# Kernel optimization log

Hardware: AMD Instinct MI355X
Metric: run time of the kernel (lower is better)

## Reference

```python
import jax, jax.numpy as jnp
import numpy as np

N_NODES = 40000
N_EDGES = 640000
IN_CH = 128
HID = 128
OUT_CH = 16
N_GRAPHS = 64
EPS = 1e-16


def segment_softmax(logits, seg, num_segments):
    m = jax.ops.segment_max(logits, seg, num_segments=num_segments)
    e = jnp.exp(logits - m[seg])
    s = jax.ops.segment_sum(e, seg, num_segments=num_segments)
    return e / (s[seg] + EPS)


def gt_conv(x, src, dst, W, b, att):
    # x: [N, Cin] -> h: [N, C]
    h = x @ W + b
    s = h @ att  # [N] per-node attention score (att broadcast over rows)
    # alpha_e = <x_i, att> + <x_j, att>; x_i = target (dst), x_j = source (src)
    alpha = s[dst] + s[src]
    alpha = jax.nn.leaky_relu(alpha, negative_slope=0.2)
    # PyG code normalizes over edge_index[0] groups (source nodes)
    alpha = segment_softmax(alpha, src, x.shape[0])
    msg = h[src] * alpha[:, None]
    return jax.ops.segment_sum(msg, dst, num_segments=x.shape[0])


def gcn_conv(x, src, dst, W, b):
    n = x.shape[0]
    h = x @ W
    deg = jax.ops.segment_sum(jnp.ones_like(src, dtype=h.dtype), dst, num_segments=n)
    dinv = jnp.where(deg > 0, deg ** -0.5, 0.0)
    norm = dinv[src] * dinv[dst]
    out = jax.ops.segment_sum(h[src] * norm[:, None], dst, num_segments=n)
    return out + b


def setup_inputs() -> dict:
    key = jax.random.key(0)
    ks = jax.random.split(key, 12)
    x = jax.random.normal(ks[0], (N_NODES, IN_CH), dtype=jnp.float32)
    edge_index = jax.random.randint(ks[1], (2, N_EDGES), 0, N_NODES, dtype=jnp.int32)
    batch = jnp.sort(jax.random.randint(ks[2], (N_NODES,), 0, N_GRAPHS, dtype=jnp.int32))
    def glorot(k, shape):
        fan_in, fan_out = shape[0], shape[-1]
        lim = jnp.sqrt(6.0 / (fan_in + fan_out))
        return jax.random.uniform(k, shape, jnp.float32, -lim, lim)
    return {
        "x": x, "edge_index": edge_index, "batch": batch,
        "W1": glorot(ks[3], (IN_CH, HID)), "b1": jnp.zeros((HID,), jnp.float32),
        "att1": glorot(ks[4], (1, HID))[0],
        "W2": glorot(ks[5], (HID, HID)), "b2": jnp.zeros((HID,), jnp.float32),
        "att2": glorot(ks[6], (1, HID))[0],
        "Wg": glorot(ks[7], (HID, HID)), "bg": jnp.zeros((HID,), jnp.float32),
        "Wfc": glorot(ks[8], (HID, OUT_CH)), "bfc": jnp.zeros((OUT_CH,), jnp.float32),
    }


def reference(x, edge_index, batch, W1, b1, att1, W2, b2, att2, Wg, bg, Wfc, bfc):
    n = x.shape[0]
    loops = jnp.arange(n, dtype=edge_index.dtype)
    src = jnp.concatenate([edge_index[0], loops])
    dst = jnp.concatenate([edge_index[1], loops])
    # two GT layers (dropout is identity in eval mode)
    h = jax.nn.relu(gt_conv(x, src, dst, W1, b1, att1))
    h = jax.nn.relu(gt_conv(h, src, dst, W2, b2, att2))
    # GCNConv (with self loops, symmetric normalization)
    h = gcn_conv(h, src, dst, Wg, bg)
    # global mean pool over graphs
    sums = jax.ops.segment_sum(h, batch, num_segments=N_GRAPHS)
    counts = jax.ops.segment_sum(jnp.ones((n,), h.dtype), batch, num_segments=N_GRAPHS)
    pooled = sums / jnp.maximum(counts, 1.0)[:, None]
    logits = pooled @ Wfc + bfc
    return jax.nn.log_softmax(logits, axis=1)
```

## Files before the change

kernel.cpp:

```cpp
#include <hip/hip_runtime.h>
#include <hip/hip_fp16.h>
#include <hip/hip_fp8.h>
#include <math.h>

#define NN 40000
#define NE 640000
#define ET 680000
#define CH 128
#define OC 16
#define NG 64
#define NQ (ET/4)
#define CAP 48
#define NBKT 8
#define BKT_DIV 5000
#define NFILLB 5320
#define NGEMMB 625
#define NGRP 79
#define GRP 72
#define NBLK1 (NGRP*GRP + (NFILLB - NGRP*64))

typedef _Float16 h8 __attribute__((ext_vector_type(8)));
typedef float    f4 __attribute__((ext_vector_type(4)));

__device__ __forceinline__ float2 fp8x2_to_f32(unsigned short v) {
    __hip_fp8_e4m3 a, b;
    a.__x = (__hip_fp8_storage_t)(v & 0xff);
    b.__x = (__hip_fp8_storage_t)(v >> 8);
    return make_float2((float)a, (float)b);
}
__device__ __forceinline__ unsigned char f32_to_fp8(float f) {
    __hip_fp8_e4m3 t(f);
    return (unsigned char)t.__x;
}

__global__ __launch_bounds__(256)
void prep(const int* __restrict__ batch, int* __restrict__ gstart,
          int* __restrict__ cur_d, int* __restrict__ cur_s,
          float* __restrict__ pooled,
          const float* __restrict__ W1, const float* __restrict__ W2,
          const float* __restrict__ Wg, _Float16* __restrict__ Wt1,
          _Float16* __restrict__ Wt2, _Float16* __restrict__ Wtg)
{
    int i = blockIdx.x * 256 + threadIdx.x;
    if (i < NN) {
        cur_d[i] = 0; cur_s[i] = 0;
        int b = batch[i];
        if (i == 0) { for (int g = 0; g <= b; ++g) gstart[g] = 0; }
        else { int pb = batch[i - 1]; for (int g = pb + 1; g <= b; ++g) gstart[g] = i; }
        if (i == NN - 1) { for (int g = b + 1; g <= NG; ++g) gstart[g] = NN; }
    }
    if (i < NG * CH) pooled[i] = 0.f;
    if (i < CH * CH) {
        int k = i >> 7, n = i & 127;
        Wt1[n * CH + k] = (_Float16)W1[i];
        Wt2[n * CH + k] = (_Float16)W2[i];
        Wtg[n * CH + k] = (_Float16)Wg[i];
    }
}

template<bool RELU, bool BIAS, bool ATTN, bool IN16>
__device__ __forceinline__
void gemm_tile(_Float16 (*xs)[136], const void* __restrict__ in_,
               const _Float16* __restrict__ Wt, const float* __restrict__ bias,
               const float* __restrict__ att, unsigned char* __restrict__ out8,
               float* __restrict__ s, int rb, int tid)
{
    if (IN16) {
        const __half* in = (const __half*)in_;
#pragma unroll
        for (int i = 0; i < 4; ++i) {
            int f = tid + i * 256;
            int r = f >> 4, c8 = f & 15;
            float4 raw = *(const float4*)(in + (size_t)(rb + r) * CH + c8 * 8);
            if (RELU) {
                __half2* h2 = (__half2*)&raw;
#pragma unroll
                for (int u = 0; u < 4; ++u) {
                    float2 fv = __half22float2(h2[u]);
                    h2[u] = __floats2half2_rn(fmaxf(fv.x, 0.f), fmaxf(fv.y, 0.f));
                }
            }
            *(float4*)&xs[r][c8 * 8] = raw;
        }
    } else {
        const float* in = (const float*)in_;
#pragma unroll
        for (int i = 0; i < 4; ++i) {
            int f = tid + i * 256;
            int r = f >> 4, c8 = f & 15;
            const float* p = in + (size_t)(rb + r) * CH + c8 * 8;
            float4 v0 = *(const float4*)p;
            float4 v1 = *(const float4*)(p + 4);
            if (RELU) {
                v0.x=fmaxf(v0.x,0.f); v0.y=fmaxf(v0.y,0.f); v0.z=fmaxf(v0.z,0.f); v0.w=fmaxf(v0.w,0.f);
                v1.x=fmaxf(v1.x,0.f); v1.y=fmaxf(v1.y,0.f); v1.z=fmaxf(v1.z,0.f); v1.w=fmaxf(v1.w,0.f);
            }
            __half2 h[4] = { __floats2half2_rn(v0.x, v0.y), __floats2half2_rn(v0.z, v0.w),
                             __floats2half2_rn(v1.x, v1.y), __floats2half2_rn(v1.z, v1.w) };
            *(float4*)&xs[r][c8 * 8] = *(float4*)h;
        }
    }
    __syncthreads();
    const int wv = tid >> 6, lane = tid & 63;
    const int m = lane & 15, quad = lane >> 4;
    f4 acc[8] = {};
    const _Float16* wp = Wt + (size_t)m * CH + quad * 8;
#pragma unroll
    for (int ks = 0; ks < 4; ++ks) {
        h8 a = *(const h8*)&xs[wv * 16 + m][ks * 32 + quad * 8];
#pragma unroll
        for (int t = 0; t < 8; ++t) {
            h8 b = *(const h8*)(wp + (size_t)t * 16 * CH + ks * 32);
            acc[t] = __builtin_amdgcn_mfma_f32_16x16x32_f16(a, b, acc[t], 0, 0, 0);
        }
    }
    float pr[4] = {0.f, 0.f, 0.f, 0.f};
#pragma unroll
    for (int t = 0; t < 8; ++t) {
        int col = t * 16 + m;
        float bv = BIAS ? bias[col] : 0.f;
        float av = ATTN ? att[col] : 0.f;
#pragma unroll
        for (int r = 0; r < 4; ++r) {
            float o = acc[t][r] + bv;
            int row = rb + wv * 16 + quad * 4 + r;
            out8[(size_t)row * CH + col] = f32_to_fp8(o);
            if (ATTN) pr[r] += o * av;
        }
    }
    if (ATTN) {
#pragma unroll
        for (int r = 0; r < 4; ++r) {
            float p = pr[r];
            p += __shfl_xor(p, 1); p += __shfl_xor(p, 2);
            p += __shfl_xor(p, 4); p += __shfl_xor(p, 8);
            if (m == 0) s[rb + wv * 16 + quad * 4 + r] = p;
        }
    }
}

__device__ __forceinline__
void fill_body(int fb, int tid, const int* __restrict__ ei,
               int* __restrict__ cur_d, int* __restrict__ cur_s,
               unsigned short* __restrict__ pad_src,
               unsigned short* __restrict__ pad_dst)
{
    int bkt = fb & (NBKT - 1);
    int q = (fb >> 3) * 256 + tid;
    if (q >= NQ) return;
    int e0 = q * 4;
    int4 sv, dv;
    if (e0 < NE) {
        sv = *(const int4*)(ei + e0);
        dv = *(const int4*)(ei + NE + e0);
    } else {
        int b = e0 - NE;
        sv = make_int4(b, b + 1, b + 2, b + 3);
        dv = sv;
    }
    const int* sc = (const int*)&sv;
    const int* dc = (const int*)&dv;
#pragma unroll
    for (int u = 0; u < 4; ++u) {
        int srcE = sc[u], dstE = dc[u];
        if ((unsigned)dstE / BKT_DIV == (unsigned)bkt) {
            int p = atomicAdd(cur_d + dstE, 1);
            if (p < CAP) pad_src[dstE * CAP + p] = (unsigned short)srcE;
        }
        if ((unsigned)srcE / BKT_DIV == (unsigned)bkt) {
            int p = atomicAdd(cur_s + srcE, 1);
            if (p < CAP) pad_dst[srcE * CAP + p] = (unsigned short)dstE;
        }
    }
}

__global__ __launch_bounds__(256)
void fill_gemm1(const float* __restrict__ x, const _Float16* __restrict__ Wt1,
                const float* __restrict__ b1, const float* __restrict__ att1,
                unsigned char* __restrict__ A8, float* __restrict__ s1,
                const int* __restrict__ ei, int* __restrict__ cur_d,
                int* __restrict__ cur_s, unsigned short* __restrict__ pad_src,
                unsigned short* __restrict__ pad_dst)
{
    __shared__ __attribute__((aligned(16))) _Float16 xs[64][136];
    int grp = blockIdx.x / GRP, o = blockIdx.x % GRP;
    if (grp < NGRP && o < 8) {
        int g = grp * 8 + o;
        if (g < NGEMMB)
            gemm_tile<false, true, true, false>(xs, x, Wt1, b1, att1,
                                                A8, s1, g * 64, threadIdx.x);
        return;
    }
    int fb = (grp < NGRP) ? grp * 64 + (o - 8)
                          : NGRP * 64 + (blockIdx.x - NGRP * GRP);
    if (fb < NFILLB)
        fill_body(fb, threadIdx.x, ei, cur_d, cur_s, pad_src, pad_dst);
}

template<bool RELU, bool BIAS, bool ATTN, bool IN16>
__global__ __launch_bounds__(256)
void gemm_k(const void* __restrict__ in_, const _Float16* __restrict__ Wt,
            const float* __restrict__ bias, const float* __restrict__ att,
            unsigned char* __restrict__ out8, float* __restrict__ s)
{
    __shared__ __attribute__((aligned(16))) _Float16 xs[64][136];
    gemm_tile<RELU, BIAS, ATTN, IN16>(xs, in_, Wt, bias, att, out8, s,
                                      blockIdx.x * 64, threadIdx.x);
}

__global__ __launch_bounds__(256)
void softmax_stats(const int* __restrict__ cur_s,
                   const unsigned short* __restrict__ pad_dst,
                   const float* __restrict__ s, float* __restrict__ ssum)
{
    int node = (blockIdx.x * 256 + threadIdx.x) >> 6;
    int lane = threadIdx.x & 63;
    if (node >= NN) return;
    int deg = min(cur_s[node], CAP);
    float si = s[node];
    float sum = 0.f;
    if (lane < deg) {
        int d = pad_dst[node * CAP + lane];
        float t = si + s[d];
        t = t > 0.f ? t : 0.2f * t;
        sum = expf(t);
    }
#pragma unroll
    for (int o = 32; o; o >>= 1) sum += __shfl_xor(sum, o);
    if (lane == 0) ssum[node] = sum;
}

__device__ __forceinline__
void gather_core(int node, int lane, int deg, int src, float w,
                 const unsigned char* __restrict__ h8p, __half* __restrict__ out16)
{
    int qtr = lane >> 4, cl = lane & 15;
    float a[8] = {};
    for (int base = 0; base < deg; base += 8) {
        uint2 v[2]; float wj[2];
#pragma unroll
        for (int u = 0; u < 2; ++u) {
            int e = base + 4 * u + qtr;
            int sj = __shfl(src, e);
            wj[u]  = __shfl(w, e);
            v[u] = ((const uint2*)(h8p + (size_t)sj * CH))[cl];
        }
#pragma unroll
        for (int u = 0; u < 2; ++u) {
            float2 p0 = fp8x2_to_f32((unsigned short)(v[u].x & 0xffff));
            float2 p1 = fp8x2_to_f32((unsigned short)(v[u].x >> 16));
            float2 p2 = fp8x2_to_f32((unsigned short)(v[u].y & 0xffff));
            float2 p3 = fp8x2_to_f32((unsigned short)(v[u].y >> 16));
            a[0] += p0.x * wj[u]; a[1] += p0.y * wj[u];
            a[2] += p1.x * wj[u]; a[3] += p1.y * wj[u];
            a[4] += p2.x * wj[u]; a[5] += p2.y * wj[u];
            a[6] += p3.x * wj[u]; a[7] += p3.y * wj[u];
        }
    }
#pragma unroll
    for (int k = 0; k < 8; ++k) {
        a[k] += __shfl_xor(a[k], 16);
        a[k] += __shfl_xor(a[k], 32);
    }
    if (qtr == 0) {
        float4 st;
        ((__half2*)&st)[0] = __floats2half2_rn(a[0], a[1]);
        ((__half2*)&st)[1] = __floats2half2_rn(a[2], a[3]);
        ((__half2*)&st)[2] = __floats2half2_rn(a[4], a[5]);
        ((__half2*)&st)[3] = __floats2half2_rn(a[6], a[7]);
        ((float4*)(out16 + (size_t)node * CH))[cl] = st;
    }
}

__global__ __launch_bounds__(256)
void gt_gather(const int* __restrict__ cur_d,
               const unsigned short* __restrict__ pad_src,
               const unsigned char* __restrict__ h8p, const float* __restrict__ s,
               const float* __restrict__ ssum, __half* __restrict__ out16)
{
    int node = (blockIdx.x * 256 + threadIdx.x) >> 6;
    int lane = threadIdx.x & 63;
    if (node >= NN) return;
    int deg = min(cur_d[node], CAP);
    float sd = s[node];
    int src = 0; float w = 0.f;
    if (lane < deg) {
        src = pad_src[node * CAP + lane];
        float t = sd + s[src];
        t = t > 0.f ? t : 0.2f * t;
        w = expf(t) / ssum[src];
    }
    gather_core(node, lane, deg, src, w, h8p, out16);
}

__global__ __launch_bounds__(256)
void gcn_gather(const int* __restrict__ cur_d,
                const unsigned short* __restrict__ pad_src,
                const unsigned char* __restrict__ h8p, __half* __restrict__ out16)
{
    int node = (blockIdx.x * 256 + threadIdx.x) >> 6;
    int lane = threadIdx.x & 63;
    if (node >= NN) return;
    int dn = cur_d[node];
    int deg = min(dn, CAP);
    float nu = rsqrtf((float)max(dn, 1));
    int src = 0; float w = 0.f;
    if (lane < deg) {
        src = pad_src[node * CAP + lane];
        w = rsqrtf((float)max(cur_d[src], 1)) * nu;
    }
    gather_core(node, lane, deg, src, w, h8p, out16);
}

__global__ __launch_bounds__(128)
void pool_part(const __half* __restrict__ h16, const int* __restrict__ batch,
               float* __restrict__ pooled)
{
    int ch = threadIdx.x;
    int start = blockIdx.x * 80;
    float acc = 0.f;
    int curg = batch[start];
    for (int base = start; base < start + 80; base += 8) {
        float vals[8]; int gs[8];
#pragma unroll
        for (int u = 0; u < 8; ++u)
            vals[u] = __half2float(h16[(size_t)(base + u) * CH + ch]);
#pragma unroll
        for (int u = 0; u < 8; ++u) gs[u] = batch[base + u];
#pragma unroll
        for (int u = 0; u < 8; ++u) {
            if (gs[u] != curg) {
                atomicAdd(pooled + (size_t)curg * CH + ch, acc);
                acc = 0.f; curg = gs[u];
            }
            acc += vals[u];
        }
    }
    atomicAdd(pooled + (size_t)curg * CH + ch, acc);
}

__global__ __launch_bounds__(256)
void head_kernel(const float* __restrict__ psum, const int* __restrict__ gstart,
                 const float* __restrict__ bg, const float* __restrict__ Wfc,
                 const float* __restrict__ bfc, float* __restrict__ out)
{
    __shared__ float lg[NG][OC];
    int tid = threadIdx.x;
#pragma unroll
    for (int i = 0; i < 4; ++i) {
        int f = tid + i * 256;
        int g = f >> 4, o = f & 15;
        float cnt = fmaxf((float)(gstart[g + 1] - gstart[g]), 1.0f);
        float inv = 1.0f / cnt;
        float acc = bfc[o];
        for (int c = 0; c < CH; ++c)
            acc += (psum[g * CH + c] * inv + bg[c]) * Wfc[c * OC + o];
        lg[g][o] = acc;
    }
    __syncthreads();
    if (tid < NG) {
        float m = -1e30f;
#pragma unroll
        for (int o = 0; o < OC; ++o) m = fmaxf(m, lg[tid][o]);
        float sum = 0.f;
#pragma unroll
        for (int o = 0; o < OC; ++o) sum += expf(lg[tid][o] - m);
        float lse = m + logf(sum);
#pragma unroll
        for (int o = 0; o < OC; ++o) out[tid * OC + o] = lg[tid][o] - lse;
    }
}

extern "C" void kernel_launch(void* const* d_in, const int* in_sizes, int n_in,
                              void* d_out, int out_size, void* d_ws, size_t ws_size,
                              hipStream_t stream)
{
    const float* x     = (const float*)d_in[0];
    const int*   ei    = (const int*)d_in[1];
    const int*   batch = (const int*)d_in[2];
    const float* W1    = (const float*)d_in[3];
    const float* b1    = (const float*)d_in[4];
    const float* att1  = (const float*)d_in[5];
    const float* W2    = (const float*)d_in[6];
    const float* b2    = (const float*)d_in[7];
    const float* att2  = (const float*)d_in[8];
    const float* Wg    = (const float*)d_in[9];
    const float* bg    = (const float*)d_in[10];
    const float* Wfc   = (const float*)d_in[11];
    const float* bfc   = (const float*)d_in[12];
    float* out = (float*)d_out;

    const size_t NNCH = (size_t)NN * CH;
    __half* B16 = (__half*)d_ws;
    unsigned char* A8 = (unsigned char*)(B16 + NNCH);
    _Float16* Wt1 = (_Float16*)(A8 + NNCH);
    _Float16* Wt2 = Wt1 + CH * CH;
    _Float16* Wtg = Wt2 + CH * CH;
    int*   cur_d  = (int*)(Wtg + CH * CH);
    int*   cur_s  = cur_d + NN;
    float* s1     = (float*)(cur_s + NN);
    float* s2     = s1 + NN;
    float* pooled = s2 + NN;
    float* ssum   = pooled + NG * CH;
    int*   gstart = (int*)(ssum + NN);
    unsigned short* pad_src = (unsigned short*)(gstart + NG + 1);
    unsigned short* pad_dst = pad_src + (size_t)NN * CAP;

    const int WB = NN / 4;

    prep<<<157, 256, 0, stream>>>(batch, gstart, cur_d, cur_s, pooled,
                                  W1, W2, Wg, Wt1, Wt2, Wtg);

    fill_gemm1<<<NBLK1, 256, 0, stream>>>(
        x, Wt1, b1, att1, A8, s1, ei, cur_d, cur_s, pad_src, pad_dst);
    softmax_stats<<<WB, 256, 0, stream>>>(cur_s, pad_dst, s1, ssum);
    gt_gather<<<WB, 256, 0, stream>>>(cur_d, pad_src, A8, s1, ssum, B16);

    gemm_k<true, true, true, true><<<NGEMMB, 256, 0, stream>>>(
        B16, Wt2, b2, att2, A8, s2);
    softmax_stats<<<WB, 256, 0, stream>>>(cur_s, pad_dst, s2, ssum);
    gt_gather<<<WB, 256, 0, stream>>>(cur_d, pad_src, A8, s2, ssum, B16);

    gemm_k<true, false, false, true><<<NGEMMB, 256, 0, stream>>>(
        B16, Wtg, nullptr, nullptr, A8, nullptr);
    gcn_gather<<<WB, 256, 0, stream>>>(cur_d, pad_src, A8, B16);

    pool_part<<<500, 128, 0, stream>>>(B16, batch, pooled);
    head_kernel<<<1, 256, 0, stream>>>(pooled, gstart, bg, Wfc, bfc, out);
}
```

Measured before the change: 293.1 us.

## Fuse attention gather into following GEMM and GCN gather into pooling

```diff
diff --git a/kernel.cpp b/kernel.cpp
--- a/kernel.cpp
+++ b/kernel.cpp
@@ -58,49 +58,13 @@
     }
 }
 
-template<bool RELU, bool BIAS, bool ATTN, bool IN16>
+template<bool BIAS, bool ATTN>
 __device__ __forceinline__
-void gemm_tile(_Float16 (*xs)[136], const void* __restrict__ in_,
-               const _Float16* __restrict__ Wt, const float* __restrict__ bias,
-               const float* __restrict__ att, unsigned char* __restrict__ out8,
-               float* __restrict__ s, int rb, int tid)
-{
-    if (IN16) {
-        const __half* in = (const __half*)in_;
-#pragma unroll
-        for (int i = 0; i < 4; ++i) {
-            int f = tid + i * 256;
-            int r = f >> 4, c8 = f & 15;
-            float4 raw = *(const float4*)(in + (size_t)(rb + r) * CH + c8 * 8);
-            if (RELU) {
-                __half2* h2 = (__half2*)&raw;
-#pragma unroll
-                for (int u = 0; u < 4; ++u) {
-                    float2 fv = __half22float2(h2[u]);
-                    h2[u] = __floats2half2_rn(fmaxf(fv.x, 0.f), fmaxf(fv.y, 0.f));
-                }
-            }
-            *(float4*)&xs[r][c8 * 8] = raw;
-        }
-    } else {
-        const float* in = (const float*)in_;
-#pragma unroll
-        for (int i = 0; i < 4; ++i) {
-            int f = tid + i * 256;
-            int r = f >> 4, c8 = f & 15;
-            const float* p = in + (size_t)(rb + r) * CH + c8 * 8;
-            float4 v0 = *(const float4*)p;
-            float4 v1 = *(const float4*)(p + 4);
-            if (RELU) {
-                v0.x=fmaxf(v0.x,0.f); v0.y=fmaxf(v0.y,0.f); v0.z=fmaxf(v0.z,0.f); v0.w=fmaxf(v0.w,0.f);
-                v1.x=fmaxf(v1.x,0.f); v1.y=fmaxf(v1.y,0.f); v1.z=fmaxf(v1.z,0.f); v1.w=fmaxf(v1.w,0.f);
-            }
-            __half2 h[4] = { __floats2half2_rn(v0.x, v0.y), __floats2half2_rn(v0.z, v0.w),
-                             __floats2half2_rn(v1.x, v1.y), __floats2half2_rn(v1.z, v1.w) };
-            *(float4*)&xs[r][c8 * 8] = *(float4*)h;
-        }
-    }
-    __syncthreads();
+void mfma_body(_Float16 (*xs)[136], const _Float16* __restrict__ Wt,
+               const float* __restrict__ bias, const float* __restrict__ att,
+               unsigned char* __restrict__ out8, float* __restrict__ s,
+               int rb, int tid)
+{
     const int wv = tid >> 6, lane = tid & 63;
     const int m = lane & 15, quad = lane >> 4;
     f4 acc[8] = {};
@@ -177,7 +141,7 @@
 __global__ __launch_bounds__(256)
 void fill_gemm1(const float* __restrict__ x, const _Float16* __restrict__ Wt1,
                 const float* __restrict__ b1, const float* __restrict__ att1,
-                unsigned char* __restrict__ A8, float* __restrict__ s1,
+                unsigned char* __restrict__ out8, float* __restrict__ s1,
                 const int* __restrict__ ei, int* __restrict__ cur_d,
                 int* __restrict__ cur_s, unsigned short* __restrict__ pad_src,
                 unsigned short* __restrict__ pad_dst)
@@ -186,26 +150,28 @@
     int grp = blockIdx.x / GRP, o = blockIdx.x % GRP;
     if (grp < NGRP && o < 8) {
         int g = grp * 8 + o;
-        if (g < NGEMMB)
-            gemm_tile<false, true, true, false>(xs, x, Wt1, b1, att1,
-                                                A8, s1, g * 64, threadIdx.x);
+        if (g < NGEMMB) {
+            int rb = g * 64, tid = threadIdx.x;
+#pragma unroll
+            for (int i = 0; i < 4; ++i) {
+                int f = tid + i * 256;
+                int r = f >> 4, c8 = f & 15;
+                const float* p = x + (size_t)(rb + r) * CH + c8 * 8;
+                float4 v0 = *(const float4*)p;
+                float4 v1 = *(const float4*)(p + 4);
+                __half2 h[4] = { __floats2half2_rn(v0.x, v0.y), __floats2half2_rn(v0.z, v0.w),
+                                 __floats2half2_rn(v1.x, v1.y), __floats2half2_rn(v1.z, v1.w) };
+                *(float4*)&xs[r][c8 * 8] = *(float4*)h;
+            }
+            __syncthreads();
+            mfma_body<true, true>(xs, Wt1, b1, att1, out8, s1, rb, tid);
+        }
         return;
     }
     int fb = (grp < NGRP) ? grp * 64 + (o - 8)
                           : NGRP * 64 + (blockIdx.x - NGRP * GRP);
     if (fb < NFILLB)
         fill_body(fb, threadIdx.x, ei, cur_d, cur_s, pad_src, pad_dst);
-}
-
-template<bool RELU, bool BIAS, bool ATTN, bool IN16>
-__global__ __launch_bounds__(256)
-void gemm_k(const void* __restrict__ in_, const _Float16* __restrict__ Wt,
-            const float* __restrict__ bias, const float* __restrict__ att,
-            unsigned char* __restrict__ out8, float* __restrict__ s)
-{
-    __shared__ __attribute__((aligned(16))) _Float16 xs[64][136];
-    gemm_tile<RELU, BIAS, ATTN, IN16>(xs, in_, Wt, bias, att, out8, s,
-                                      blockIdx.x * 64, threadIdx.x);
 }
 
 __global__ __launch_bounds__(256)
@@ -230,113 +196,139 @@
     if (lane == 0) ssum[node] = sum;
 }
 
-__device__ __forceinline__
-void gather_core(int node, int lane, int deg, int src, float w,
-                 const unsigned char* __restrict__ h8p, __half* __restrict__ out16)
-{
-    int qtr = lane >> 4, cl = lane & 15;
-    float a[8] = {};
-    for (int base = 0; base < deg; base += 8) {
-        uint2 v[2]; float wj[2];
-#pragma unroll
-        for (int u = 0; u < 2; ++u) {
-            int e = base + 4 * u + qtr;
-            int sj = __shfl(src, e);
-            wj[u]  = __shfl(w, e);
-            v[u] = ((const uint2*)(h8p + (size_t)sj * CH))[cl];
-        }
-#pragma unroll
-        for (int u = 0; u < 2; ++u) {
-            float2 p0 = fp8x2_to_f32((unsigned short)(v[u].x & 0xffff));
-            float2 p1 = fp8x2_to_f32((unsigned short)(v[u].x >> 16));
-            float2 p2 = fp8x2_to_f32((unsigned short)(v[u].y & 0xffff));
-            float2 p3 = fp8x2_to_f32((unsigned short)(v[u].y >> 16));
-            a[0] += p0.x * wj[u]; a[1] += p0.y * wj[u];
-            a[2] += p1.x * wj[u]; a[3] += p1.y * wj[u];
-            a[4] += p2.x * wj[u]; a[5] += p2.y * wj[u];
-            a[6] += p3.x * wj[u]; a[7] += p3.y * wj[u];
-        }
-    }
-#pragma unroll
-    for (int k = 0; k < 8; ++k) {
-        a[k] += __shfl_xor(a[k], 16);
-        a[k] += __shfl_xor(a[k], 32);
+template<bool BIAS, bool ATTN>
+__global__ __launch_bounds__(256)
+void gather_gemm(const int* __restrict__ cur_d,
+                 const unsigned short* __restrict__ pad_src,
+                 const unsigned char* __restrict__ in8,
+                 const float* __restrict__ s_in, const float* __restrict__ ssum,
+                 const _Float16* __restrict__ Wt, const float* __restrict__ bias,
+                 const float* __restrict__ att, unsigned char* __restrict__ out8,
+                 float* __restrict__ s_out)
+{
+    __shared__ __attribute__((aligned(16))) _Float16 xs[64][136];
+    const int tid = threadIdx.x;
+    const int rb = blockIdx.x * 64;
+    const int wv = tid >> 6, lane = tid & 63;
+    const int qtr = lane >> 4, cl = lane & 15;
+    for (int i = 0; i < 16; ++i) {
+        int node = rb + wv * 16 + i;
+        int deg = min(cur_d[node], CAP);
+        int src = 0; float w = 0.f;
+        if (lane < deg) {
+            src = pad_src[node * CAP + lane];
+            float t = s_in[node] + s_in[src];
+            t = t > 0.f ? t : 0.2f * t;
+            w = expf(t) / ssum[src];
+        }
+        float a[8] = {};
+        for (int base = 0; base < deg; base += 8) {
+            uint2 v[2]; float wj[2];
+#pragma unroll
+            for (int u = 0; u < 2; ++u) {
+                int e = base + 4 * u + qtr;
+                int sj = __shfl(src, e);
+                wj[u]  = __shfl(w, e);
+                v[u] = ((const uint2*)(in8 + (size_t)sj * CH))[cl];
+            }
+#pragma unroll
+            for (int u = 0; u < 2; ++u) {
+                float2 p0 = fp8x2_to_f32((unsigned short)(v[u].x & 0xffff));
+                float2 p1 = fp8x2_to_f32((unsigned short)(v[u].x >> 16));
+                float2 p2 = fp8x2_to_f32((unsigned short)(v[u].y & 0xffff));
+                float2 p3 = fp8x2_to_f32((unsigned short)(v[u].y >> 16));
+                a[0] += p0.x * wj[u]; a[1] += p0.y * wj[u];
+                a[2] += p1.x * wj[u]; a[3] += p1.y * wj[u];
+                a[4] += p2.x * wj[u]; a[5] += p2.y * wj[u];
+                a[6] += p3.x * wj[u]; a[7] += p3.y * wj[u];
+            }
+        }
+#pragma unroll
+        for (int k = 0; k < 8; ++k) {
+            a[k] += __shfl_xor(a[k], 16);
+            a[k] += __shfl_xor(a[k], 32);
+        }
+        if (qtr == 0) {
+            float4 st;
+            ((__half2*)&st)[0] = __floats2half2_rn(fmaxf(a[0], 0.f), fmaxf(a[1], 0.f));
+            ((__half2*)&st)[1] = __floats2half2_rn(fmaxf(a[2], 0.f), fmaxf(a[3], 0.f));
+            ((__half2*)&st)[2] = __floats2half2_rn(fmaxf(a[4], 0.f), fmaxf(a[5], 0.f));
+            ((__half2*)&st)[3] = __floats2half2_rn(fmaxf(a[6], 0.f), fmaxf(a[7], 0.f));
+            *(float4*)&xs[wv * 16 + i][cl * 8] = st;
+        }
+    }
+    __syncthreads();
+    mfma_body<BIAS, ATTN>(xs, Wt, bias, att, out8, s_out, rb, tid);
+}
+
+__global__ __launch_bounds__(256)
+void gcn_pool(const int* __restrict__ cur_d,
+              const unsigned short* __restrict__ pad_src,
+              const unsigned char* __restrict__ in8,
+              const int* __restrict__ batch, float* __restrict__ pooled)
+{
+    const int tid = threadIdx.x;
+    const int rb = blockIdx.x * 64;
+    const int wv = tid >> 6, lane = tid & 63;
+    const int qtr = lane >> 4, cl = lane & 15;
+    float pacc[8] = {};
+    int curg = batch[rb + wv * 16];
+    for (int i = 0; i < 16; ++i) {
+        int node = rb + wv * 16 + i;
+        int dn = cur_d[node];
+        int deg = min(dn, CAP);
+        float nu = rsqrtf((float)max(dn, 1));
+        int src = 0; float w = 0.f;
+        if (lane < deg) {
+            src = pad_src[node * CAP + lane];
+            w = rsqrtf((float)max(cur_d[src], 1)) * nu;
+        }
+        float a[8] = {};
+        for (int base = 0; base < deg; base += 8) {
+            uint2 v[2]; float wj[2];
+#pragma unroll
+            for (int u = 0; u < 2; ++u) {
+                int e = base + 4 * u + qtr;
+                int sj = __shfl(src, e);
+                wj[u]  = __shfl(w, e);
+                v[u] = ((const uint2*)(in8 + (size_t)sj * CH))[cl];
+            }
+#pragma unroll
+            for (int u = 0; u < 2; ++u) {
+                float2 p0 = fp8x2_to_f32((unsigned short)(v[u].x & 0xffff));
+                float2 p1 = fp8x2_to_f32((unsigned short)(v[u].x >> 16));
+                float2 p2 = fp8x2_to_f32((unsigned short)(v[u].y & 0xffff));
+                float2 p3 = fp8x2_to_f32((unsigned short)(v[u].y >> 16));
+                a[0] += p0.x * wj[u]; a[1] += p0.y * wj[u];
+                a[2] += p1.x * wj[u]; a[3] += p1.y * wj[u];
+                a[4] += p2.x * wj[u]; a[5] += p2.y * wj[u];
+                a[6] += p3.x * wj[u]; a[7] += p3.y * wj[u];
+            }
+        }
+#pragma unroll
+        for (int k = 0; k < 8; ++k) {
+            a[k] += __shfl_xor(a[k], 16);
+            a[k] += __shfl_xor(a[k], 32);
+        }
+        int g = batch[node];
+        if (g != curg) {
+            if (qtr == 0) {
+#pragma unroll
+                for (int k = 0; k < 8; ++k)
+                    atomicAdd(pooled + (size_t)curg * CH + cl * 8 + k, pacc[k]);
+            }
+#pragma unroll
+            for (int k = 0; k < 8; ++k) pacc[k] = 0.f;
+            curg = g;
+        }
+#pragma unroll
+        for (int k = 0; k < 8; ++k) pacc[k] += a[k];
     }
     if (qtr == 0) {
-        float4 st;
-        ((__half2*)&st)[0] = __floats2half2_rn(a[0], a[1]);
-        ((__half2*)&st)[1] = __floats2half2_rn(a[2], a[3]);
-        ((__half2*)&st)[2] = __floats2half2_rn(a[4], a[5]);
-        ((__half2*)&st)[3] = __floats2half2_rn(a[6], a[7]);
-        ((float4*)(out16 + (size_t)node * CH))[cl] = st;
-    }
-}
-
-__global__ __launch_bounds__(256)
-void gt_gather(const int* __restrict__ cur_d,
-               const unsigned short* __restrict__ pad_src,
-               const unsigned char* __restrict__ h8p, const float* __restrict__ s,
-               const float* __restrict__ ssum, __half* __restrict__ out16)
-{
-    int node = (blockIdx.x * 256 + threadIdx.x) >> 6;
-    int lane = threadIdx.x & 63;
-    if (node >= NN) return;
-    int deg = min(cur_d[node], CAP);
-    float sd = s[node];
-    int src = 0; float w = 0.f;
-    if (lane < deg) {
-        src = pad_src[node * CAP + lane];
-        float t = sd + s[src];
-        t = t > 0.f ? t : 0.2f * t;
-        w = expf(t) / ssum[src];
-    }
-    gather_core(node, lane, deg, src, w, h8p, out16);
-}
-
-__global__ __launch_bounds__(256)
-void gcn_gather(const int* __restrict__ cur_d,
-                const unsigned short* __restrict__ pad_src,
-                const unsigned char* __restrict__ h8p, __half* __restrict__ out16)
-{
-    int node = (blockIdx.x * 256 + threadIdx.x) >> 6;
-    int lane = threadIdx.x & 63;
-    if (node >= NN) return;
-    int dn = cur_d[node];
-    int deg = min(dn, CAP);
-    float nu = rsqrtf((float)max(dn, 1));
-    int src = 0; float w = 0.f;
-    if (lane < deg) {
-        src = pad_src[node * CAP + lane];
-        w = rsqrtf((float)max(cur_d[src], 1)) * nu;
-    }
-    gather_core(node, lane, deg, src, w, h8p, out16);
-}
-
-__global__ __launch_bounds__(128)
-void pool_part(const __half* __restrict__ h16, const int* __restrict__ batch,
-               float* __restrict__ pooled)
-{
-    int ch = threadIdx.x;
-    int start = blockIdx.x * 80;
-    float acc = 0.f;
-    int curg = batch[start];
-    for (int base = start; base < start + 80; base += 8) {
-        float vals[8]; int gs[8];
-#pragma unroll
-        for (int u = 0; u < 8; ++u)
-            vals[u] = __half2float(h16[(size_t)(base + u) * CH + ch]);
-#pragma unroll
-        for (int u = 0; u < 8; ++u) gs[u] = batch[base + u];
-#pragma unroll
-        for (int u = 0; u < 8; ++u) {
-            if (gs[u] != curg) {
-                atomicAdd(pooled + (size_t)curg * CH + ch, acc);
-                acc = 0.f; curg = gs[u];
-            }
-            acc += vals[u];
-        }
-    }
-    atomicAdd(pooled + (size_t)curg * CH + ch, acc);
+#pragma unroll
+        for (int k = 0; k < 8; ++k)
+            atomicAdd(pooled + (size_t)curg * CH + cl * 8 + k, pacc[k]);
+    }
 }
 
 __global__ __launch_bounds__(256)
@@ -391,9 +383,9 @@
     float* out = (float*)d_out;
 
     const size_t NNCH = (size_t)NN * CH;
-    __half* B16 = (__half*)d_ws;
-    unsigned char* A8 = (unsigned char*)(B16 + NNCH);
-    _Float16* Wt1 = (_Float16*)(A8 + NNCH);
+    unsigned char* P = (unsigned char*)d_ws;
+    unsigned char* Q = P + NNCH;
+    _Float16* Wt1 = (_Float16*)(Q + NNCH);
     _Float16* Wt2 = Wt1 + CH * CH;
     _Float16* Wtg = Wt2 + CH * CH;
     int*   cur_d  = (int*)(Wtg + CH * CH);
@@ -412,19 +404,17 @@
                                   W1, W2, Wg, Wt1, Wt2, Wtg);
 
     fill_gemm1<<<NBLK1, 256, 0, stream>>>(
-        x, Wt1, b1, att1, A8, s1, ei, cur_d, cur_s, pad_src, pad_dst);
+        x, Wt1, b1, att1, P, s1, ei, cur_d, cur_s, pad_src, pad_dst);
     softmax_stats<<<WB, 256, 0, stream>>>(cur_s, pad_dst, s1, ssum);
-    gt_gather<<<WB, 256, 0, stream>>>(cur_d, pad_src, A8, s1, ssum, B16);
-
-    gemm_k<true, true, true, true><<<NGEMMB, 256, 0, stream>>>(
-        B16, Wt2, b2, att2, A8, s2);
+
+    gather_gemm<true, true><<<NGEMMB, 256, 0, stream>>>(
+        cur_d, pad_src, P, s1, ssum, Wt2, b2, att2, Q, s2);
     softmax_stats<<<WB, 256, 0, stream>>>(cur_s, pad_dst, s2, ssum);
-    gt_gather<<<WB, 256, 0, stream>>>(cur_d, pad_src, A8, s2, ssum, B16);
-
-    gemm_k<true, false, false, true><<<NGEMMB, 256, 0, stream>>>(
-        B16, Wtg, nullptr, nullptr, A8, nullptr);
-    gcn_gather<<<WB, 256, 0, stream>>>(cur_d, pad_src, A8, B16);
-
-    pool_part<<<500, 128, 0, stream>>>(B16, batch, pooled);
+
+    gather_gemm<false, false><<<NGEMMB, 256, 0, stream>>>(
+        cur_d, pad_src, Q, s2, ssum, Wtg, nullptr, nullptr, P, nullptr);
+
+    gcn_pool<<<NGEMMB, 256, 0, stream>>>(cur_d, pad_src, P, batch, pooled);
+
     head_kernel<<<1, 256, 0, stream>>>(pooled, gstart, bg, Wfc, bfc, out);
 }
```

Result: slower. 338.5 us (+15.5%).
